# Performance work log

Measured on AMD Instinct MI355X. Metric: run time of the kernel, lower is better.

The kernel has to match this reference:

```python
import jax, jax.numpy as jnp
import numpy as np

B, S, I, H, C, V = 512, 64, 300, 1024, 2, 50000


def setup_inputs() -> dict:
    key = jax.random.key(0)
    ks = jax.random.split(key, 10)
    s = 0.05
    return {
        "x": jax.random.randint(ks[0], (B, S), 0, V),
        "lengths": jax.random.randint(ks[1], (B,), 1, S + 1),
        "embed": jax.random.normal(ks[2], (V, I), jnp.float32) * s,
        "Wih_e": jax.random.normal(ks[3], (4 * H, I), jnp.float32) * s,
        "Whh_e": jax.random.normal(ks[4], (4 * H, H), jnp.float32) * s,
        "bih_e": jnp.zeros((4 * H,), jnp.float32),
        "bhh_e": jnp.zeros((4 * H,), jnp.float32),
        "Wih_d": jax.random.normal(ks[5], (4 * H, I), jnp.float32) * s,
        "Whh_d": jax.random.normal(ks[6], (4 * H, H), jnp.float32) * s,
        "bih_d": jnp.zeros((4 * H,), jnp.float32),
        "bhh_d": jnp.zeros((4 * H,), jnp.float32),
        "W_lin": jax.random.normal(ks[7], (C, H), jnp.float32) * s,
        "b_lin": jnp.zeros((C,), jnp.float32),
    }


def lstm_cell(xi, h, c, Wih, Whh, bih, bhh):
    # PyTorch LSTMCell gate order: i, f, g, o
    g = xi @ Wih.T + bih + h @ Whh.T + bhh
    i, f, gg, o = jnp.split(g, 4, axis=-1)
    c = jax.nn.sigmoid(f) * c + jax.nn.sigmoid(i) * jnp.tanh(gg)
    return jax.nn.sigmoid(o) * jnp.tanh(c), c


def reference(x, lengths, embed, Wih_e, Whh_e, bih_e, bhh_e,
              Wih_d, Whh_d, bih_d, bhh_d, W_lin, b_lin):
    bsz, slen = x.shape
    hdim = Whh_e.shape[1]
    ncls = W_lin.shape[0]
    xs = embed[x.T]                      # [S, B, I] (seq-major, like x.transpose(0,1))

    h0 = jnp.zeros((bsz, hdim), xs.dtype)
    c0 = jnp.zeros((bsz, hdim), xs.dtype)

    def enc_step(carry, xi):
        h, c = carry
        h, c = lstm_cell(xi, h, c, Wih_e, Whh_e, bih_e, bhh_e)
        return (h, c), h

    # forward pass over sequence
    (h, c), enc_fwd = jax.lax.scan(enc_step, (h0, c0), xs)          # enc_fwd: [S,B,H]
    # backward pass with the SAME encoder cell, continuing from (h, c)
    (h, c), h_bwd = jax.lax.scan(enc_step, (h, c), xs[::-1])        # h_bwd:  [S,B,H]
    # k-th backward step pairs with encoder_forward[k] in the original code
    enc_out = (enc_fwd + h_bwd) * 0.5                               # [S,B,H]

    def dec_step(carry, xi):
        h, c = carry
        # original attention sums over batch AND hidden -> one scalar per timestep,
        # and rebuilds w as a fresh Variable (no gradient through the weights).
        w = jax.nn.softmax(jnp.sum(h[None, :, :] * enc_out, axis=(1, 2)))  # [S]
        w = jax.lax.stop_gradient(w)
        h = h + jnp.einsum('t,tbh->bh', w, enc_out)
        h, c = lstm_cell(xi, h, c, Wih_d, Whh_d, bih_d, bhh_d)
        return (h, c), h

    _, dec = jax.lax.scan(dec_step, (h, c), xs)                     # [S,B,H]

    out = dec @ W_lin.T + b_lin                                     # [S,B,C]
    out = out.transpose(1, 0, 2)                                    # [B,S,C]
    pad = jnp.array([1.0, 0.0], out.dtype)                          # overwrite beyond lengths
    mask = jnp.arange(slen)[None, :] < lengths[:, None]             # [B,S]
    out = jnp.where(mask[:, :, None], out, pad)
    return out.reshape(bsz * slen, ncls)
```

## Files before the change

kernel.cpp:

```cpp
#include <hip/hip_runtime.h>
#include <hip/hip_bf16.h>

#define BSZ 512
#define SEQ 64
#define IDIM 300
#define KP1 384
#define HDIM 1024
#define G4 4096
#define BH (BSZ*HDIM)

typedef __attribute__((ext_vector_type(8))) short bf16x8;
typedef __attribute__((ext_vector_type(4))) float f32x4;
typedef __attribute__((ext_vector_type(8))) unsigned short u16x8;
typedef __attribute__((ext_vector_type(4))) unsigned short u16x4;

__device__ __forceinline__ float sigmoidf_(float x){ return 1.f/(1.f+__expf(-x)); }
__device__ __forceinline__ float bf2f(unsigned short u){
    union{unsigned int i; float f;} v; v.i = ((unsigned)u)<<16; return v.f;
}
__device__ __forceinline__ unsigned short f2bf(float f){
    __hip_bfloat16 b = __float2bfloat16(f);
    return *(unsigned short*)&b;
}

__global__ void embed_gather_k(const int* __restrict__ x, const float* __restrict__ embed,
                               __hip_bfloat16* __restrict__ xs){
    int t = blockIdx.x, b = blockIdx.y;
    int ix = x[b*SEQ + t];
    const float* src = embed + (size_t)ix * IDIM;
    __hip_bfloat16* dst = xs + ((size_t)t*BSZ + b) * KP1;
    for (int k = threadIdx.x; k < KP1; k += 64)
        dst[k] = __float2bfloat16(k < IDIM ? src[k] : 0.f);
}

__global__ void conv_w_k(const float* __restrict__ Wih_e, const float* __restrict__ Wih_d,
                         const float* __restrict__ Whh_e, const float* __restrict__ Whh_d,
                         __hip_bfloat16* __restrict__ Pe, __hip_bfloat16* __restrict__ Pd,
                         __hip_bfloat16* __restrict__ He, __hip_bfloat16* __restrict__ Hd){
    int nr = blockIdx.x, v = blockIdx.y;
    int orig = ((nr>>5)&3)*HDIM + (nr>>7)*32 + (nr&31);
    if (v < 2){
        const float* src = (v ? Wih_d : Wih_e) + (size_t)orig*IDIM;
        __hip_bfloat16* dst = (v ? Pd : Pe) + (size_t)nr*KP1;
        for (int k = threadIdx.x; k < KP1; k += 64)
            dst[k] = __float2bfloat16(k < IDIM ? src[k] : 0.f);
    } else {
        const float* src = ((v == 3) ? Whh_d : Whh_e) + (size_t)orig*HDIM;
        __hip_bfloat16* dst = ((v == 3) ? Hd : He) + (size_t)nr*HDIM;
        for (int k = threadIdx.x; k < HDIM; k += 64)
            dst[k] = __float2bfloat16(src[k]);
    }
}

__global__ void bias_comb_k(const float* __restrict__ a, const float* __restrict__ b2,
                            const float* __restrict__ c2, const float* __restrict__ d2,
                            float* __restrict__ be, float* __restrict__ bd){
    int i = blockIdx.x*256 + threadIdx.x;
    int nr = i & 4095;
    int orig = ((nr>>5)&3)*HDIM + (nr>>7)*32 + (nr&31);
    if (i < G4) be[nr] = a[orig] + b2[orig];
    else        bd[nr] = c2[orig] + d2[orig];
}

__global__ void zero_hc_k(float* __restrict__ h, float* __restrict__ c,
                          __hip_bfloat16* __restrict__ h_bf){
    int idx = blockIdx.x*256 + threadIdx.x;
    h[idx] = 0.f; c[idx] = 0.f; h_bf[idx] = __float2bfloat16(0.f);
}

#define BM 64
#define BN 128
#define NK1 (KP1/128)
#define NK2 (HDIM/128)
#define NKT (NK1+NK2)

__global__ __launch_bounds__(512) void xpre_k(
    const __hip_bfloat16* __restrict__ xs, const __hip_bfloat16* __restrict__ B1,
    float* __restrict__ Gx)
{
    __shared__ __align__(16) char smem[131072];
    const int tid  = threadIdx.x;
    const int lane = tid & 63, wv = tid >> 6;
    const int row0 = blockIdx.y * BM;
    const int col0 = blockIdx.x * BN;
    const int wm = wv >> 2, wn = wv & 3;
    const int fb = blockIdx.y*32 + blockIdx.x;

    #pragma unroll
    for (int ks = 0; ks < 3; ++ks)
        #pragma unroll
        for (int q = 0; q < 4; ++q){
            int u = q*512 + tid;
            int r = u >> 4, s = u & 15;
            int g = s ^ (r & 15);
            const __hip_bfloat16* src = B1 + (size_t)(col0 + r)*KP1 + ks*128 + g*8;
            char* dst = smem + ks*32768 + q*8192 + wv*1024;
            __builtin_amdgcn_global_load_lds(
                (const __attribute__((address_space(1))) void*)src,
                (__attribute__((address_space(3))) void*)dst, 16, 0, 0);
        }

    auto stage_a = [&](int t, int ks, int p){
        #pragma unroll
        for (int half = 0; half < 2; ++half){
            int u = half*512 + tid;
            int r = u >> 4, s = u & 15;
            int g = s ^ (r & 15);
            const __hip_bfloat16* src = xs + (size_t)t*BSZ*KP1 + (size_t)(row0 + r)*KP1 + ks*128 + g*8;
            char* dst = smem + 98304 + p*16384 + half*8192 + wv*1024;
            __builtin_amdgcn_global_load_lds(
                (const __attribute__((address_space(1))) void*)src,
                (__attribute__((address_space(3))) void*)dst, 16, 0, 0);
        }
    };

    f32x4 acc[2][2] = {};
    auto compute_a = [&](int p, int ks){
        const char* Ab = smem + 98304 + p*16384;
        const char* Bb = smem + ks*32768;
        const int rr = lane & 15, g = lane >> 4;
        bf16x8 af[2][4], bfr[2][4];
        #pragma unroll
        for (int m = 0; m < 2; ++m){
            int r = wm*32 + m*16 + rr;
            #pragma unroll
            for (int kk = 0; kk < 4; ++kk)
                af[m][kk] = *(const bf16x8*)(Ab + r*256 + ((kk*4 + g) ^ (r & 15))*16);
        }
        #pragma unroll
        for (int n = 0; n < 2; ++n){
            int r = wn*32 + n*16 + rr;
            #pragma unroll
            for (int kk = 0; kk < 4; ++kk)
                bfr[n][kk] = *(const bf16x8*)(Bb + r*256 + ((kk*4 + g) ^ (r & 15))*16);
        }
        #pragma unroll
        for (int kk = 0; kk < 4; ++kk)
            #pragma unroll
            for (int m = 0; m < 2; ++m)
                #pragma unroll
                for (int n = 0; n < 2; ++n)
                    acc[m][n] = __builtin_amdgcn_mfma_f32_16x16x32_bf16(af[m][kk], bfr[n][kk], acc[m][n], 0, 0, 0);
    };

    stage_a(0, 0, 0);
    __syncthreads();
    for (int t = 0; t < SEQ; ++t){
        #pragma unroll
        for (int ks = 0; ks < 3; ++ks){
            int u = t*3 + ks;
            int p = u & 1;
            if (u + 1 < SEQ*3) stage_a((u+1)/3, (u+1)%3, p ^ 1);
            compute_a(p, ks);
            if (ks == 2){
                float* gp = Gx + (((size_t)t*256 + fb)*512 + tid)*16;
                #pragma unroll
                for (int m = 0; m < 2; ++m)
                    #pragma unroll
                    for (int n = 0; n < 2; ++n)
                        *(f32x4*)(gp + (m*2+n)*4) = acc[m][n];
                acc[0][0] = f32x4{}; acc[0][1] = f32x4{};
                acc[1][0] = f32x4{}; acc[1][1] = f32x4{};
            }
            __syncthreads();
        }
    }
}

template<int XPRE>
__global__ __launch_bounds__(512) void lstm_step_k(
    const __hip_bfloat16* __restrict__ A1, const __hip_bfloat16* __restrict__ B1,
    const __hip_bfloat16* __restrict__ A2, const __hip_bfloat16* __restrict__ B2,
    const float* __restrict__ bias, const float* __restrict__ Gxt,
    float* __restrict__ c, float* __restrict__ h, __hip_bfloat16* __restrict__ h_bf,
    __hip_bfloat16* __restrict__ encSlot, int mode)
{
    constexpr int NKT_ = XPRE ? NK2 : NKT;
    __shared__ __align__(16) char smem[98304];
    const int tid  = threadIdx.x;
    const int lane = tid & 63, wv = tid >> 6;
    const int row0 = blockIdx.y * BM;
    const int col0 = blockIdx.x * BN;
    const int wm = wv >> 2, wn = wv & 3;

    f32x4 acc[2][2];
    if constexpr (XPRE){
        const float* gp = Gxt + (((size_t)(blockIdx.y*32 + blockIdx.x))*512 + tid)*16;
        #pragma unroll
        for (int m = 0; m < 2; ++m)
            #pragma unroll
            for (int n = 0; n < 2; ++n)
                acc[m][n] = *(const f32x4*)(gp + (m*2+n)*4);
    } else {
        acc[0][0] = f32x4{}; acc[0][1] = f32x4{};
        acc[1][0] = f32x4{}; acc[1][1] = f32x4{};
    }

    auto stage = [&](int ks, int p){
        const __hip_bfloat16* A; const __hip_bfloat16* B; int KA, k0;
        if constexpr (XPRE){ A = A2; B = B2; KA = HDIM; k0 = ks*128; }
        else {
            if (ks < NK1){ A = A1; B = B1; KA = KP1;  k0 = ks*128; }
            else         { A = A2; B = B2; KA = HDIM; k0 = (ks-NK1)*128; }
        }
        char* base = smem + p*49152;
        #pragma unroll
        for (int half = 0; half < 2; ++half){
            int u = half*512 + tid;
            int r = u >> 4, s = u & 15;
            int g = s ^ (r & 15);
            const __hip_bfloat16* src = A + (size_t)(row0 + r)*KA + k0 + g*8;
            char* dst = base + half*8192 + wv*1024;
            __builtin_amdgcn_global_load_lds(
                (const __attribute__((address_space(1))) void*)src,
                (__attribute__((address_space(3))) void*)dst, 16, 0, 0);
        }
        #pragma unroll
        for (int q = 0; q < 4; ++q){
            int u = q*512 + tid;
            int r = u >> 4, s = u & 15;
            int g = s ^ (r & 15);
            const __hip_bfloat16* src = B + (size_t)(col0 + r)*KA + k0 + g*8;
            char* dst = base + 16384 + q*8192 + wv*1024;
            __builtin_amdgcn_global_load_lds(
                (const __attribute__((address_space(1))) void*)src,
                (__attribute__((address_space(3))) void*)dst, 16, 0, 0);
        }
    };

    auto compute = [&](int p){
        const char* Ab = smem + p*49152;
        const char* Bb = Ab + 16384;
        const int rr = lane & 15, g = lane >> 4;
        bf16x8 af[2][4], bfr[2][4];
        #pragma unroll
        for (int m = 0; m < 2; ++m){
            int r = wm*32 + m*16 + rr;
            #pragma unroll
            for (int kk = 0; kk < 4; ++kk)
                af[m][kk] = *(const bf16x8*)(Ab + r*256 + ((kk*4 + g) ^ (r & 15))*16);
        }
        #pragma unroll
        for (int n = 0; n < 2; ++n){
            int r = wn*32 + n*16 + rr;
            #pragma unroll
            for (int kk = 0; kk < 4; ++kk)
                bfr[n][kk] = *(const bf16x8*)(Bb + r*256 + ((kk*4 + g) ^ (r & 15))*16);
        }
        #pragma unroll
        for (int kk = 0; kk < 4; ++kk)
            #pragma unroll
            for (int m = 0; m < 2; ++m)
                #pragma unroll
                for (int n = 0; n < 2; ++n)
                    acc[m][n] = __builtin_amdgcn_mfma_f32_16x16x32_bf16(af[m][kk], bfr[n][kk], acc[m][n], 0, 0, 0);
    };

    const int erow = tid >> 3;
    const int ejj0 = (tid & 7) * 4;
    const size_t ebase = (size_t)(row0 + erow)*HDIM + blockIdx.x*32 + ejj0;

    stage(0, 0);
    const f32x4 cpre = *(const f32x4*)(c + ebase);
    __syncthreads();
    for (int ks = 0; ks < NKT_; ++ks){
        int p = ks & 1;
        if (ks + 1 < NKT_) stage(ks + 1, p ^ 1);
        compute(p);
        __syncthreads();
    }

    float* ep = (float*)smem;
    {
        const int rr = lane & 15, q4 = lane >> 4;
        #pragma unroll
        for (int m = 0; m < 2; ++m){
            int row = wm*32 + m*16 + q4*4;
            #pragma unroll
            for (int n = 0; n < 2; ++n){
                int jj = n*16 + rr;
                float bi = bias[col0 + wn*32 + jj];
                #pragma unroll
                for (int q = 0; q < 4; ++q)
                    ep[(wn*64 + row + q)*33 + jj] = acc[m][n][q] + bi;
            }
        }
    }
    __syncthreads();
    {
        f32x4 cv, hv;
        #pragma unroll
        for (int e = 0; e < 4; ++e){
            float gi = ep[(0*64 + erow)*33 + ejj0 + e];
            float gf = ep[(1*64 + erow)*33 + ejj0 + e];
            float gg = ep[(2*64 + erow)*33 + ejj0 + e];
            float go = ep[(3*64 + erow)*33 + ejj0 + e];
            float cc = sigmoidf_(gf)*cpre[e] + sigmoidf_(gi)*tanhf(gg);
            float hh = sigmoidf_(go)*tanhf(cc);
            cv[e] = cc; hv[e] = hh;
        }
        *(f32x4*)(c + ebase) = cv;
        *(f32x4*)(h + ebase) = hv;
        u16x4 hb;
        #pragma unroll
        for (int e = 0; e < 4; ++e) hb[e] = f2bf(hv[e]);
        *(u16x4*)(h_bf + ebase) = hb;
        if (mode == 0){
            *(u16x4*)(encSlot + ebase) = hb;
        } else if (mode == 1){
            u16x4 eo = *(const u16x4*)(encSlot + ebase);
            u16x4 r;
            #pragma unroll
            for (int e = 0; e < 4; ++e) r[e] = f2bf(0.5f*(bf2f(eo[e]) + hv[e]));
            *(u16x4*)(encSlot + ebase) = r;
        }
    }
}

__global__ __launch_bounds__(256) void attn_part_k(
    const __hip_bfloat16* __restrict__ h_bf, const __hip_bfloat16* __restrict__ enc,
    float* __restrict__ part,
    const float* __restrict__ h, const float* __restrict__ Wl, const float* __restrict__ bl,
    const int* __restrict__ len, float* __restrict__ out, int dect)
{
    __shared__ float red[4];
    int lane = threadIdx.x & 63, w = threadIdx.x >> 6;
    if (blockIdx.x < 64){
        int ch = blockIdx.x;
        int s  = blockIdx.y;
        const u16x8* e  = (const u16x8*)(enc + (size_t)s*BH + (size_t)ch*8192);
        const u16x8* hp = (const u16x8*)(h_bf + (size_t)ch*8192);
        float sum = 0.f;
        for (int i = threadIdx.x; i < 1024; i += 256){
            u16x8 ev = e[i], hv = hp[i];
            #pragma unroll
            for (int j = 0; j < 8; ++j) sum += bf2f(hv[j]) * bf2f(ev[j]);
        }
        #pragma unroll
        for (int m = 32; m >= 1; m >>= 1) sum += __shfl_xor(sum, m);
        if (lane == 0) red[w] = sum;
        __syncthreads();
        if (threadIdx.x == 0) part[s*64 + ch] = red[0]+red[1]+red[2]+red[3];
    } else if (dect >= 0){
        int b = ((blockIdx.x - 64)*64 + blockIdx.y)*4 + w;
        const float* hb = h + (size_t)b*HDIM;
        float s0 = 0.f, s1 = 0.f;
        for (int j = lane; j < HDIM; j += 64){
            float v = hb[j];
            s0 += v * Wl[j];
            s1 += v * Wl[HDIM + j];
        }
        #pragma unroll
        for (int m = 32; m >= 1; m >>= 1){ s0 += __shfl_xor(s0, m); s1 += __shfl_xor(s1, m); }
        if (lane == 0){
            bool valid = dect < len[b];
            size_t r = ((size_t)b*SEQ + dect)*2;
            out[r]   = valid ? (s0 + bl[0]) : 1.0f;
            out[r+1] = valid ? (s1 + bl[1]) : 0.0f;
        }
    }
}

__global__ __launch_bounds__(256) void attn_apply_k(
    const float* __restrict__ h, const float* __restrict__ part,
    const __hip_bfloat16* __restrict__ enc, __hip_bfloat16* __restrict__ hat_bf)
{
    __shared__ float wl[64];
    int lane = threadIdx.x & 63;
    if (threadIdx.x < 64){
        float tot = 0.f;
        #pragma unroll 8
        for (int ch = 0; ch < 64; ++ch) tot += part[lane*64 + ch];
        float m = tot;
        #pragma unroll
        for (int msk = 32; msk >= 1; msk >>= 1) m = fmaxf(m, __shfl_xor(m, msk));
        float e = __expf(tot - m);
        float sm = e;
        #pragma unroll
        for (int msk = 32; msk >= 1; msk >>= 1) sm += __shfl_xor(sm, msk);
        wl[lane] = e / sm;
    }
    __syncthreads();
    size_t i4 = ((size_t)blockIdx.x*256 + threadIdx.x) * 4;
    float v[4];
    {
        f32x4 a = *(const f32x4*)(h + i4);
        v[0]=a[0]; v[1]=a[1]; v[2]=a[2]; v[3]=a[3];
    }
    for (int s = 0; s < SEQ; ++s){
        u16x4 ev = *(const u16x4*)(enc + (size_t)s*BH + i4);
        float w = wl[s];
        #pragma unroll
        for (int j = 0; j < 4; ++j) v[j] += w * bf2f(ev[j]);
    }
    u16x4 ov;
    #pragma unroll
    for (int j = 0; j < 4; ++j) ov[j] = f2bf(v[j]);
    *(u16x4*)(hat_bf + i4) = ov;
}

__global__ void dec_linear_k(const float* __restrict__ h, const float* __restrict__ Wl,
                             const float* __restrict__ bl, const int* __restrict__ len,
                             float* __restrict__ out, int t)
{
    int b = blockIdx.x, lane = threadIdx.x;
    const float* hb = h + (size_t)b*HDIM;
    float s0 = 0.f, s1 = 0.f;
    for (int j = lane; j < HDIM; j += 64){
        float v = hb[j];
        s0 += v * Wl[j];
        s1 += v * Wl[HDIM + j];
    }
    #pragma unroll
    for (int m = 32; m >= 1; m >>= 1){ s0 += __shfl_xor(s0, m); s1 += __shfl_xor(s1, m); }
    if (lane == 0){
        bool valid = t < len[b];
        size_t r = ((size_t)b*SEQ + t)*2;
        out[r]   = valid ? (s0 + bl[0]) : 1.0f;
        out[r+1] = valid ? (s1 + bl[1]) : 0.0f;
    }
}

extern "C" void kernel_launch(void* const* d_in, const int* in_sizes, int n_in,
                              void* d_out, int out_size, void* d_ws, size_t ws_size,
                              hipStream_t stream)
{
    (void)in_sizes; (void)n_in; (void)out_size;
    const int*   x      = (const int*)  d_in[0];
    const int*   len    = (const int*)  d_in[1];
    const float* embed  = (const float*)d_in[2];
    const float* Wih_e  = (const float*)d_in[3];
    const float* Whh_e  = (const float*)d_in[4];
    const float* bih_e  = (const float*)d_in[5];
    const float* bhh_e  = (const float*)d_in[6];
    const float* Wih_d  = (const float*)d_in[7];
    const float* Whh_d  = (const float*)d_in[8];
    const float* bih_d  = (const float*)d_in[9];
    const float* bhh_d  = (const float*)d_in[10];
    const float* W_lin  = (const float*)d_in[11];
    const float* b_lin  = (const float*)d_in[12];
    float* out = (float*)d_out;

    float* ws = (float*)d_ws;
    size_t off = 0;
    auto alloc = [&](size_t nfloats){ size_t o = off; off += (nfloats + 63) & ~(size_t)63; return o; };
    __hip_bfloat16* xs_bf  = (__hip_bfloat16*)(ws + alloc((size_t)SEQ*BSZ*KP1/2));
    __hip_bfloat16* Pe     = (__hip_bfloat16*)(ws + alloc((size_t)G4*KP1/2));
    __hip_bfloat16* Pd     = (__hip_bfloat16*)(ws + alloc((size_t)G4*KP1/2));
    __hip_bfloat16* He     = (__hip_bfloat16*)(ws + alloc((size_t)G4*HDIM/2));
    __hip_bfloat16* Hd     = (__hip_bfloat16*)(ws + alloc((size_t)G4*HDIM/2));
    float* be   = ws + alloc(G4);
    float* bd   = ws + alloc(G4);
    float* h    = ws + alloc(BH);
    float* c    = ws + alloc(BH);
    __hip_bfloat16* h_bf   = (__hip_bfloat16*)(ws + alloc(BH/2));
    __hip_bfloat16* hat_bf = (__hip_bfloat16*)(ws + alloc(BH/2));
    __hip_bfloat16* enc    = (__hip_bfloat16*)(ws + alloc((size_t)SEQ*BH/2));
    float* part = ws + alloc(64*64);
    float* Gx   = ws + alloc((size_t)SEQ*256*512*16);
    const bool useGx = (off * sizeof(float)) <= ws_size;

    embed_gather_k<<<dim3(SEQ, BSZ), 64, 0, stream>>>(x, embed, xs_bf);
    conv_w_k<<<dim3(G4, 4), 64, 0, stream>>>(Wih_e, Wih_d, Whh_e, Whh_d, Pe, Pd, He, Hd);
    bias_comb_k<<<32, 256, 0, stream>>>(bih_e, bhh_e, bih_d, bhh_d, be, bd);
    zero_hc_k<<<BH/256, 256, 0, stream>>>(h, c, h_bf);
    if (useGx)
        xpre_k<<<dim3(32, 8), 512, 0, stream>>>(xs_bf, Pe, Gx);

    dim3 ggrid(G4/BN, BSZ/BM);
    const size_t gxstep = (size_t)256*512*16;

    for (int t = 0; t < SEQ; ++t){
        if (useGx)
            lstm_step_k<1><<<ggrid, 512, 0, stream>>>(xs_bf + (size_t)t*BSZ*KP1, Pe, h_bf, He, be,
                                                      Gx + (size_t)t*gxstep,
                                                      c, h, h_bf, enc + (size_t)t*BH, 0);
        else
            lstm_step_k<0><<<ggrid, 512, 0, stream>>>(xs_bf + (size_t)t*BSZ*KP1, Pe, h_bf, He, be,
                                                      nullptr, c, h, h_bf, enc + (size_t)t*BH, 0);
    }
    for (int k = 0; k < SEQ; ++k){
        int t = SEQ - 1 - k;
        if (useGx)
            lstm_step_k<1><<<ggrid, 512, 0, stream>>>(xs_bf + (size_t)t*BSZ*KP1, Pe, h_bf, He, be,
                                                      Gx + (size_t)t*gxstep,
                                                      c, h, h_bf, enc + (size_t)k*BH, 1);
        else
            lstm_step_k<0><<<ggrid, 512, 0, stream>>>(xs_bf + (size_t)t*BSZ*KP1, Pe, h_bf, He, be,
                                                      nullptr, c, h, h_bf, enc + (size_t)k*BH, 1);
    }
    for (int t = 0; t < SEQ; ++t){
        attn_part_k<<<dim3(66, 64), 256, 0, stream>>>(h_bf, enc, part, h, W_lin, b_lin, len, out, t - 1);
        attn_apply_k<<<512, 256, 0, stream>>>(h, part, enc, hat_bf);
        lstm_step_k<0><<<ggrid, 512, 0, stream>>>(xs_bf + (size_t)t*BSZ*KP1, Pd, hat_bf, Hd, bd,
                                                  nullptr, c, h, h_bf, nullptr, 2);
    }
    dec_linear_k<<<BSZ, 64, 0, stream>>>(h, W_lin, b_lin, len, out, SEQ - 1);
}
```

Baseline: 4.336 ms.

## Fuse encoder recurrence into one persistent kernel with a software grid barrier

Replaces the 128 per-step encoder launches with a single persistent kernel of 256 blocks that loops over both encoder passes. Blocks synchronise with an atomic generation-counter grid barrier, and the cell state stays in registers across steps. The goal is to remove kernel-launch overhead and the global round-trips for c between steps. The barrier assumes all 256 blocks are co-resident (launch bounds of 2 blocks per CU with 96KB LDS each), so it risks deadlock if occupancy falls short, and the spin barrier adds its own per-step latency.

```diff
diff --git a/kernel.cpp b/kernel.cpp
--- a/kernel.cpp
+++ b/kernel.cpp
@@ -63,9 +63,11 @@
 }
 
 __global__ void zero_hc_k(float* __restrict__ h, float* __restrict__ c,
-                          __hip_bfloat16* __restrict__ h_bf){
+                          __hip_bfloat16* __restrict__ h_bf,
+                          unsigned int* __restrict__ bar, unsigned int* __restrict__ gen){
     int idx = blockIdx.x*256 + threadIdx.x;
     h[idx] = 0.f; c[idx] = 0.f; h_bf[idx] = __float2bfloat16(0.f);
+    if (idx == 0){ bar[0] = 0u; gen[0] = 0u; }
 }
 
 #define BM 64
@@ -164,6 +166,170 @@
             }
             __syncthreads();
         }
+    }
+}
+
+__device__ __forceinline__ void grid_sync_(unsigned int* bar, unsigned int* gen){
+    __syncthreads();
+    __threadfence();
+    if (threadIdx.x == 0){
+        unsigned int g = __hip_atomic_load(gen, __ATOMIC_RELAXED, __HIP_MEMORY_SCOPE_AGENT);
+        if (__hip_atomic_fetch_add(bar, 1u, __ATOMIC_ACQ_REL, __HIP_MEMORY_SCOPE_AGENT) == 255u){
+            __hip_atomic_store(bar, 0u, __ATOMIC_RELAXED, __HIP_MEMORY_SCOPE_AGENT);
+            __hip_atomic_fetch_add(gen, 1u, __ATOMIC_RELEASE, __HIP_MEMORY_SCOPE_AGENT);
+        } else {
+            while (__hip_atomic_load(gen, __ATOMIC_ACQUIRE, __HIP_MEMORY_SCOPE_AGENT) == g)
+                __builtin_amdgcn_s_sleep(2);
+        }
+    }
+    __syncthreads();
+    __threadfence();
+}
+
+__global__ __launch_bounds__(512, 2) void enc_persist_k(
+    const __hip_bfloat16* __restrict__ B2, const float* __restrict__ bias,
+    const float* __restrict__ Gx,
+    float* __restrict__ c, float* __restrict__ h, __hip_bfloat16* __restrict__ h_bf,
+    __hip_bfloat16* __restrict__ enc,
+    unsigned int* __restrict__ bar, unsigned int* __restrict__ gen)
+{
+    __shared__ __align__(16) char smem[98304];
+    const int tid  = threadIdx.x;
+    const int lane = tid & 63, wv = tid >> 6;
+    const int bid  = blockIdx.x;
+    const int bx = bid & 31, by = bid >> 5;
+    const int row0 = by * BM;
+    const int col0 = bx * BN;
+    const int wm = wv >> 2, wn = wv & 3;
+
+    const int erow = tid >> 3;
+    const int ejj0 = (tid & 7) * 4;
+    const size_t ebase = (size_t)(row0 + erow)*HDIM + bx*32 + ejj0;
+
+    f32x4 creg = {0.f, 0.f, 0.f, 0.f};
+
+    auto stage = [&](int ks, int p){
+        char* base = smem + p*49152;
+        #pragma unroll
+        for (int half = 0; half < 2; ++half){
+            int u = half*512 + tid;
+            int r = u >> 4, s = u & 15;
+            int g = s ^ (r & 15);
+            const __hip_bfloat16* src = h_bf + (size_t)(row0 + r)*HDIM + ks*128 + g*8;
+            char* dst = base + half*8192 + wv*1024;
+            __builtin_amdgcn_global_load_lds(
+                (const __attribute__((address_space(1))) void*)src,
+                (__attribute__((address_space(3))) void*)dst, 16, 0, 0);
+        }
+        #pragma unroll
+        for (int q = 0; q < 4; ++q){
+            int u = q*512 + tid;
+            int r = u >> 4, s = u & 15;
+            int g = s ^ (r & 15);
+            const __hip_bfloat16* src = B2 + (size_t)(col0 + r)*HDIM + ks*128 + g*8;
+            char* dst = base + 16384 + q*8192 + wv*1024;
+            __builtin_amdgcn_global_load_lds(
+                (const __attribute__((address_space(1))) void*)src,
+                (__attribute__((address_space(3))) void*)dst, 16, 0, 0);
+        }
+    };
+
+    for (int i = 0; i < 2*SEQ; ++i){
+        const int t = (i < SEQ) ? i : (2*SEQ - 1 - i);
+        f32x4 acc[2][2];
+        {
+            const float* gp = Gx + (((size_t)t*256 + bid)*512 + tid)*16;
+            #pragma unroll
+            for (int m = 0; m < 2; ++m)
+                #pragma unroll
+                for (int n = 0; n < 2; ++n)
+                    acc[m][n] = *(const f32x4*)(gp + (m*2+n)*4);
+        }
+
+        stage(0, 0);
+        __syncthreads();
+        for (int ks = 0; ks < NK2; ++ks){
+            int p = ks & 1;
+            if (ks + 1 < NK2) stage(ks + 1, p ^ 1);
+            {
+                const char* Ab = smem + p*49152;
+                const char* Bb = Ab + 16384;
+                const int rr = lane & 15, g = lane >> 4;
+                bf16x8 af[2][4], bfr[2][4];
+                #pragma unroll
+                for (int m = 0; m < 2; ++m){
+                    int r = wm*32 + m*16 + rr;
+                    #pragma unroll
+                    for (int kk = 0; kk < 4; ++kk)
+                        af[m][kk] = *(const bf16x8*)(Ab + r*256 + ((kk*4 + g) ^ (r & 15))*16);
+                }
+                #pragma unroll
+                for (int n = 0; n < 2; ++n){
+                    int r = wn*32 + n*16 + rr;
+                    #pragma unroll
+                    for (int kk = 0; kk < 4; ++kk)
+                        bfr[n][kk] = *(const bf16x8*)(Bb + r*256 + ((kk*4 + g) ^ (r & 15))*16);
+                }
+                #pragma unroll
+                for (int kk = 0; kk < 4; ++kk)
+                    #pragma unroll
+                    for (int m = 0; m < 2; ++m)
+                        #pragma unroll
+                        for (int n = 0; n < 2; ++n)
+                            acc[m][n] = __builtin_amdgcn_mfma_f32_16x16x32_bf16(af[m][kk], bfr[n][kk], acc[m][n], 0, 0, 0);
+            }
+            __syncthreads();
+        }
+
+        float* ep = (float*)smem;
+        {
+            const int rr = lane & 15, q4 = lane >> 4;
+            #pragma unroll
+            for (int m = 0; m < 2; ++m){
+                int row = wm*32 + m*16 + q4*4;
+                #pragma unroll
+                for (int n = 0; n < 2; ++n){
+                    int jj = n*16 + rr;
+                    float bi = bias[col0 + wn*32 + jj];
+                    #pragma unroll
+                    for (int q = 0; q < 4; ++q)
+                        ep[(wn*64 + row + q)*33 + jj] = acc[m][n][q] + bi;
+                }
+            }
+        }
+        __syncthreads();
+        {
+            f32x4 hv;
+            #pragma unroll
+            for (int e = 0; e < 4; ++e){
+                float gi = ep[(0*64 + erow)*33 + ejj0 + e];
+                float gf = ep[(1*64 + erow)*33 + ejj0 + e];
+                float gg = ep[(2*64 + erow)*33 + ejj0 + e];
+                float go = ep[(3*64 + erow)*33 + ejj0 + e];
+                float cc = sigmoidf_(gf)*creg[e] + sigmoidf_(gi)*tanhf(gg);
+                float hh = sigmoidf_(go)*tanhf(cc);
+                creg[e] = cc; hv[e] = hh;
+            }
+            u16x4 hb;
+            #pragma unroll
+            for (int e = 0; e < 4; ++e) hb[e] = f2bf(hv[e]);
+            *(u16x4*)(h_bf + ebase) = hb;
+            if (i < SEQ){
+                *(u16x4*)(enc + (size_t)i*BH + ebase) = hb;
+            } else {
+                __hip_bfloat16* eslot = enc + (size_t)(i - SEQ)*BH;
+                u16x4 eo = *(const u16x4*)(eslot + ebase);
+                u16x4 r;
+                #pragma unroll
+                for (int e = 0; e < 4; ++e) r[e] = f2bf(0.5f*(bf2f(eo[e]) + hv[e]));
+                *(u16x4*)(eslot + ebase) = r;
+            }
+            if (i == 2*SEQ - 1){
+                *(f32x4*)(c + ebase) = creg;
+                *(f32x4*)(h + ebase) = hv;
+            }
+        }
+        grid_sync_(bar, gen);
     }
 }
 
@@ -457,38 +623,32 @@
     __hip_bfloat16* hat_bf = (__hip_bfloat16*)(ws + alloc(BH/2));
     __hip_bfloat16* enc    = (__hip_bfloat16*)(ws + alloc((size_t)SEQ*BH/2));
     float* part = ws + alloc(64*64);
+    unsigned int* bar = (unsigned int*)(ws + alloc(32));
+    unsigned int* gen = bar + 16;
     float* Gx   = ws + alloc((size_t)SEQ*256*512*16);
     const bool useGx = (off * sizeof(float)) <= ws_size;
 
     embed_gather_k<<<dim3(SEQ, BSZ), 64, 0, stream>>>(x, embed, xs_bf);
     conv_w_k<<<dim3(G4, 4), 64, 0, stream>>>(Wih_e, Wih_d, Whh_e, Whh_d, Pe, Pd, He, Hd);
     bias_comb_k<<<32, 256, 0, stream>>>(bih_e, bhh_e, bih_d, bhh_d, be, bd);
-    zero_hc_k<<<BH/256, 256, 0, stream>>>(h, c, h_bf);
-    if (useGx)
+    zero_hc_k<<<BH/256, 256, 0, stream>>>(h, c, h_bf, bar, gen);
+
+    dim3 ggrid(G4/BN, BSZ/BM);
+
+    if (useGx){
         xpre_k<<<dim3(32, 8), 512, 0, stream>>>(xs_bf, Pe, Gx);
-
-    dim3 ggrid(G4/BN, BSZ/BM);
-    const size_t gxstep = (size_t)256*512*16;
-
-    for (int t = 0; t < SEQ; ++t){
-        if (useGx)
-            lstm_step_k<1><<<ggrid, 512, 0, stream>>>(xs_bf + (size_t)t*BSZ*KP1, Pe, h_bf, He, be,
-                                                      Gx + (size_t)t*gxstep,
-                                                      c, h, h_bf, enc + (size_t)t*BH, 0);
-        else
+        enc_persist_k<<<256, 512, 0, stream>>>(He, be, Gx, c, h, h_bf, enc, bar, gen);
+    } else {
+        for (int t = 0; t < SEQ; ++t)
             lstm_step_k<0><<<ggrid, 512, 0, stream>>>(xs_bf + (size_t)t*BSZ*KP1, Pe, h_bf, He, be,
                                                       nullptr, c, h, h_bf, enc + (size_t)t*BH, 0);
-    }
-    for (int k = 0; k < SEQ; ++k){
-        int t = SEQ - 1 - k;
-        if (useGx)
-            lstm_step_k<1><<<ggrid, 512, 0, stream>>>(xs_bf + (size_t)t*BSZ*KP1, Pe, h_bf, He, be,
-                                                      Gx + (size_t)t*gxstep,
-                                                      c, h, h_bf, enc + (size_t)k*BH, 1);
-        else
+        for (int k = 0; k < SEQ; ++k){
+            int t = SEQ - 1 - k;
             lstm_step_k<0><<<ggrid, 512, 0, stream>>>(xs_bf + (size_t)t*BSZ*KP1, Pe, h_bf, He, be,
                                                       nullptr, c, h, h_bf, enc + (size_t)k*BH, 1);
-    }
+        }
+    }
+
     for (int t = 0; t < SEQ; ++t){
         attn_part_k<<<dim3(66, 64), 256, 0, stream>>>(h_bf, enc, part, h, W_lin, b_lin, len, out, t - 1);
         attn_apply_k<<<512, 256, 0, stream>>>(h, part, enc, hat_bf);
```

Result: no change. 4.341 ms (+0.1%).
